# Optimization experiments

Measured on AMD Instinct MI355X. Metric: run time of the kernel, lower is better.

## Reference

```python
import jax, jax.numpy as jnp
import numpy as np

N_NODES = 50000
N_EDGES = 150000
F_IN = 128
D = 512
N_GRAPHS = 256
BN_EPS = 1e-5


def setup_inputs() -> dict:
    key = jax.random.key(0)
    ks = jax.random.split(key, 16)
    x = jax.random.normal(ks[0], (N_NODES, F_IN), dtype=jnp.float32)
    edge_index = jax.random.randint(ks[1], (2, N_EDGES), 0, N_NODES, dtype=jnp.int64)
    batch = jnp.sort(jax.random.randint(ks[2], (N_NODES,), 0, N_GRAPHS, dtype=jnp.int64))
    # layer 1 MLP (F_IN -> D -> D)
    W1a = jax.random.normal(ks[3], (F_IN, D), dtype=jnp.float32) / np.sqrt(F_IN)
    b1a = jnp.zeros((D,), dtype=jnp.float32)
    W1b = jax.random.normal(ks[4], (D, D), dtype=jnp.float32) / np.sqrt(D)
    b1b = jnp.zeros((D,), dtype=jnp.float32)
    # layers 2-5 MLPs (D -> D -> D), stacked on leading axis
    Wa = jax.random.normal(ks[5], (4, D, D), dtype=jnp.float32) / np.sqrt(D)
    ba = jnp.zeros((4, D), dtype=jnp.float32)
    Wb = jax.random.normal(ks[6], (4, D, D), dtype=jnp.float32) / np.sqrt(D)
    bb = jnp.zeros((4, D), dtype=jnp.float32)
    # batchnorm affine params for the 5 BN layers
    gammas = jnp.ones((5, D), dtype=jnp.float32)
    betas = jnp.zeros((5, D), dtype=jnp.float32)
    # final fc
    fcW = jax.random.normal(ks[7], (D, D), dtype=jnp.float32) / np.sqrt(D)
    fcb = jnp.zeros((D,), dtype=jnp.float32)
    return {"x": x, "edge_index": edge_index, "batch": batch,
            "W1a": W1a, "b1a": b1a, "W1b": W1b, "b1b": b1b,
            "Wa": Wa, "ba": ba, "Wb": Wb, "bb": bb,
            "gammas": gammas, "betas": betas, "fcW": fcW, "fcb": fcb}


def _gin_block(x, src, dst, wa, ba_, wb, bb_, gamma, beta):
    # GINConv (eps=0): h_i = x_i + sum_{j->i} x_j, then 2-layer MLP
    agg = jnp.zeros_like(x).at[dst].add(x[src])
    h = x + agg
    h = jnp.maximum(h @ wa + ba_, 0.0) @ wb + bb_
    # outer ReLU then BatchNorm1d (training-mode batch stats, biased var)
    h = jnp.maximum(h, 0.0)
    mean = h.mean(axis=0)
    var = ((h - mean) ** 2).mean(axis=0)
    return gamma * (h - mean) * jax.lax.rsqrt(var + BN_EPS) + beta


def reference(x, edge_index, batch, W1a, b1a, W1b, b1b, Wa, ba, Wb, bb,
              gammas, betas, fcW, fcb):
    src, dst = edge_index[0], edge_index[1]
    h = _gin_block(x, src, dst, W1a, b1a, W1b, b1b, gammas[0], betas[0])
    for i in range(4):
        h = _gin_block(h, src, dst, Wa[i], ba[i], Wb[i], bb[i],
                       gammas[i + 1], betas[i + 1])
    # global mean pool over graphs
    sums = jax.ops.segment_sum(h, batch, num_segments=N_GRAPHS)
    counts = jax.ops.segment_sum(jnp.ones((h.shape[0],), dtype=h.dtype), batch,
                                 num_segments=N_GRAPHS)
    pooled = sums / jnp.maximum(counts, 1.0)[:, None]
    return jnp.tanh(pooled @ fcW + fcb)
```

## Files before the change

kernel.cpp:

```cpp
#include <hip/hip_runtime.h>
#include <math.h>

typedef unsigned short u16;
typedef unsigned int u32;
typedef __attribute__((ext_vector_type(8))) short bf16x8;
typedef __attribute__((ext_vector_type(4))) float f32x4;

__device__ __forceinline__ u16 f2bf(float x) {
    u32 u = __float_as_uint(x);
    return (u16)((u + 0x7FFFu + ((u >> 16) & 1u)) >> 16);
}
__device__ __forceinline__ float bf2f(u16 h) {
    return __uint_as_float(((u32)h) << 16);
}
__device__ __forceinline__ void async16(const void* g, void* l) {
    __builtin_amdgcn_global_load_lds((const __attribute__((address_space(1))) void*)g,
                                     (__attribute__((address_space(3))) void*)l,
                                     16, 0, 0);
}

__device__ __forceinline__ int idx_at(const void* p, long long i, int is64) {
    if (is64) return (int)((const long long*)p)[i];
    return ((const int*)p)[i];
}

__global__ void detect_kernel(const int* __restrict__ ei, int E, int* __restrict__ flag) {
    __shared__ int any;
    if (threadIdx.x == 0) any = 0;
    __syncthreads();
    int n = min(E, 1024);
    for (int i = threadIdx.x; i < n; i += blockDim.x)
        if (ei[2 * i + 1] != 0) any = 1;
    __syncthreads();
    if (threadIdx.x == 0) *flag = (any == 0) ? 1 : 0;
}

__global__ void hist_kernel(const void* __restrict__ idx, long long offs,
                            const int* __restrict__ flag,
                            int* __restrict__ cnt, int n) {
    int is64 = *flag;
    int i = blockIdx.x * blockDim.x + threadIdx.x;
    if (i < n) atomicAdd(&cnt[idx_at(idx, offs + i, is64)], 1);
}

__global__ void scan1_kernel(const int* __restrict__ cnt, int* __restrict__ ofs,
                             int* __restrict__ bsum, int n) {
    __shared__ int s[256];
    int b = blockIdx.x, t = threadIdx.x;
    int base = b * 1024 + t * 4;
    int v0 = (base + 0 < n) ? cnt[base + 0] : 0;
    int v1 = (base + 1 < n) ? cnt[base + 1] : 0;
    int v2 = (base + 2 < n) ? cnt[base + 2] : 0;
    int v3 = (base + 3 < n) ? cnt[base + 3] : 0;
    int tsum = v0 + v1 + v2 + v3;
    s[t] = tsum;
    __syncthreads();
    for (int off = 1; off < 256; off <<= 1) {
        int u = (t >= off) ? s[t - off] : 0;
        __syncthreads();
        s[t] += u;
        __syncthreads();
    }
    int pre = s[t] - tsum;
    int e0 = pre + v0, e1 = e0 + v1, e2 = e1 + v2, e3 = e2 + v3;
    if (base + 0 < n) ofs[base + 1] = e0;
    if (base + 1 < n) ofs[base + 2] = e1;
    if (base + 2 < n) ofs[base + 3] = e2;
    if (base + 3 < n) ofs[base + 4] = e3;
    if (t == 255) bsum[b] = s[255];
    if (b == 0 && t == 0) ofs[0] = 0;
}

__global__ void scan2_kernel(int* __restrict__ bsum, int nb) {
    int t = threadIdx.x;
    int orig = (t < nb) ? bsum[t] : 0;
    int v = orig;
    for (int d = 1; d < 64; d <<= 1) {
        int u = __shfl_up(v, d);
        if (t >= d) v += u;
    }
    if (t < nb) bsum[t] = v - orig;
}

__global__ void scan3_kernel(int* __restrict__ ofs, const int* __restrict__ bsum, int n) {
    int i = blockIdx.x * blockDim.x + threadIdx.x;
    if (i < n) ofs[i + 1] += bsum[i >> 10];
}

__global__ void fill_csr_kernel(const void* __restrict__ ei, long long E,
                                const int* __restrict__ flag,
                                int* __restrict__ cursor, int* __restrict__ esrc, int e) {
    int is64 = *flag;
    int i = blockIdx.x * blockDim.x + threadIdx.x;
    if (i < e) {
        int d = idx_at(ei, E + i, is64);
        int s = idx_at(ei, i, is64);
        int p = atomicAdd(&cursor[d], 1);
        esrc[p] = s;
    }
}

__global__ void copy_int_kernel(const int* __restrict__ a, int* __restrict__ b, int n) {
    int i = blockIdx.x * blockDim.x + threadIdx.x;
    if (i < n) b[i] = a[i];
}

__global__ void aggregate_split_kernel(const float* __restrict__ X,
                                       const int* __restrict__ row_ofs,
                                       const int* __restrict__ esrc,
                                       const float* __restrict__ scale,
                                       const float* __restrict__ shift,
                                       u16* __restrict__ Zhi, u16* __restrict__ Zlo,
                                       int n, int ncols) {
    int tpr = ncols >> 2;
    int nper = 256 / tpr;
    int node = blockIdx.x * nper + threadIdx.x / tpr;
    int c = (threadIdx.x % tpr) * 4;
    if (node >= n) return;
    int beg = row_ofs[node], end = row_ofs[node + 1];
    float4 acc = *reinterpret_cast<const float4*>(X + (size_t)node * ncols + c);
    int e = beg;
    for (; e + 1 < end; e += 2) {
        int s0 = esrc[e], s1 = esrc[e + 1];
        float4 a = *reinterpret_cast<const float4*>(X + (size_t)s0 * ncols + c);
        float4 b = *reinterpret_cast<const float4*>(X + (size_t)s1 * ncols + c);
        acc.x += a.x + b.x; acc.y += a.y + b.y;
        acc.z += a.z + b.z; acc.w += a.w + b.w;
    }
    if (e < end) {
        int s0 = esrc[e];
        float4 a = *reinterpret_cast<const float4*>(X + (size_t)s0 * ncols + c);
        acc.x += a.x; acc.y += a.y; acc.z += a.z; acc.w += a.w;
    }
    if (scale) {
        float d1 = (float)(end - beg + 1);
        float4 sc = *reinterpret_cast<const float4*>(scale + c);
        float4 sh = *reinterpret_cast<const float4*>(shift + c);
        acc.x = sc.x * acc.x + d1 * sh.x;
        acc.y = sc.y * acc.y + d1 * sh.y;
        acc.z = sc.z * acc.z + d1 * sh.z;
        acc.w = sc.w * acc.w + d1 * sh.w;
    }
    ushort4 hv, lv;
    hv.x = f2bf(acc.x); lv.x = f2bf(acc.x - bf2f(hv.x));
    hv.y = f2bf(acc.y); lv.y = f2bf(acc.y - bf2f(hv.y));
    hv.z = f2bf(acc.z); lv.z = f2bf(acc.z - bf2f(hv.z));
    hv.w = f2bf(acc.w); lv.w = f2bf(acc.w - bf2f(hv.w));
    *reinterpret_cast<ushort4*>(Zhi + (size_t)node * ncols + c) = hv;
    *reinterpret_cast<ushort4*>(Zlo + (size_t)node * ncols + c) = lv;
}

__global__ void transpose_split_kernel(const float* __restrict__ W, int K, int N,
                                       u16* __restrict__ Thi, u16* __restrict__ Tlo) {
    __shared__ float t[32][33];
    int k0 = blockIdx.x * 32, n0 = blockIdx.y * 32;
    int tx = threadIdx.x & 31, ty = threadIdx.x >> 5;
#pragma unroll
    for (int i = 0; i < 32; i += 8)
        t[ty + i][tx] = W[(size_t)(k0 + ty + i) * N + n0 + tx];
    __syncthreads();
#pragma unroll
    for (int i = 0; i < 32; i += 8) {
        float v = t[tx][ty + i];
        size_t o = (size_t)(n0 + ty + i) * K + k0 + tx;
        u16 h = f2bf(v);
        Thi[o] = h;
        Tlo[o] = f2bf(v - bf2f(h));
    }
}

struct TBatch {
    const float* src[10];
    u16* dh[10];
    u16* dl[10];
};
__global__ void transpose_split_batch_kernel(TBatch tb) {
    __shared__ float t[32][33];
    int z = blockIdx.z;
    const float* W = tb.src[z];
    u16* Thi = tb.dh[z];
    u16* Tlo = tb.dl[z];
    int k0 = blockIdx.x * 32, n0 = blockIdx.y * 32;
    int tx = threadIdx.x & 31, ty = threadIdx.x >> 5;
#pragma unroll
    for (int i = 0; i < 32; i += 8)
        t[ty + i][tx] = W[(size_t)(k0 + ty + i) * 512 + n0 + tx];
    __syncthreads();
#pragma unroll
    for (int i = 0; i < 32; i += 8) {
        float v = t[tx][ty + i];
        size_t o = (size_t)(n0 + ty + i) * 512 + k0 + tx;
        u16 h = f2bf(v);
        Thi[o] = h;
        Tlo[o] = f2bf(v - bf2f(h));
    }
}

template <int MODE>
__global__ __launch_bounds__(512, 2)
void gemm_mfma(const u16* __restrict__ Ahi, const u16* __restrict__ Alo,
               const u16* __restrict__ Bhi, const u16* __restrict__ Blo,
               const float* __restrict__ bias, int M, int K, int mblk,
               u16* __restrict__ Ohi, u16* __restrict__ Olo,
               float* __restrict__ Of32, float* __restrict__ stats) {
    __shared__ __align__(16) char lds[131072];

    const int bid = blockIdx.x;
    const int mt = (bid >> 5) * 8 + (bid & 7);
    const int nbk = (bid & 31) >> 3;
    if (mt >= mblk) return;
    const int row0 = mt * 128;
    const int col0 = nbk * 128;

    const int tid = threadIdx.x;
    const int lane = tid & 63;
    const int wave = tid >> 6;
    const int wr = wave >> 2, wc = wave & 3;

    f32x4 acc[4][2];
#pragma unroll
    for (int mi = 0; mi < 4; ++mi)
#pragma unroll
        for (int ni = 0; ni < 2; ++ni)
            acc[mi][ni] = (f32x4){0.f, 0.f, 0.f, 0.f};

    auto stage = [&](int buf, int kt) {
        char* ldsA = lds + buf * 65536;
        char* ldsB = ldsA + 32768;
        const int k0 = kt << 6;
#pragma unroll
        for (int i = 0; i < 4; ++i) {
            int lin = tid + i * 512;
            int row = lin >> 4, p = lin & 15;
            int c = p ^ (row & 15);
            int eo = (c & 7) * 8;
            int ar = row0 + row; if (ar > M - 1) ar = M - 1;
            const u16* asrc = (c < 8 ? Ahi : Alo) + (size_t)ar * K + k0 + eo;
            async16(asrc, ldsA + lin * 16);
            const u16* bsrc = (c < 8 ? Bhi : Blo) + (size_t)(col0 + row) * K + k0 + eo;
            async16(bsrc, ldsB + lin * 16);
        }
    };

    const int nkt = K >> 6;
    stage(0, 0);
    __syncthreads();

    int cur = 0;
    for (int kt = 0; kt < nkt; ++kt) {
        if (kt + 1 < nkt) stage(cur ^ 1, kt + 1);
        char* ldsA = lds + cur * 65536;
        char* ldsB = ldsA + 32768;
#pragma unroll
        for (int kk = 0; kk < 2; ++kk) {
            bf16x8 ah[4], al[4], bh[2], bl[2];
            const int kc = lane >> 4;
            const int chi = kk * 4 + kc;
#pragma unroll
            for (int mi = 0; mi < 4; ++mi) {
                int ml = wr * 64 + mi * 16 + (lane & 15);
                const char* base = ldsA + ml * 256;
                ah[mi] = *(const bf16x8*)(base + ((chi ^ (ml & 15)) << 4));
                al[mi] = *(const bf16x8*)(base + (((chi + 8) ^ (ml & 15)) << 4));
            }
#pragma unroll
            for (int ni = 0; ni < 2; ++ni) {
                int nl = wc * 32 + ni * 16 + (lane & 15);
                const char* base = ldsB + nl * 256;
                bh[ni] = *(const bf16x8*)(base + ((chi ^ (nl & 15)) << 4));
                bl[ni] = *(const bf16x8*)(base + (((chi + 8) ^ (nl & 15)) << 4));
            }
            __builtin_amdgcn_s_setprio(1);
#pragma unroll
            for (int mi = 0; mi < 4; ++mi)
#pragma unroll
                for (int ni = 0; ni < 2; ++ni) {
                    acc[mi][ni] = __builtin_amdgcn_mfma_f32_16x16x32_bf16(
                        ah[mi], bh[ni], acc[mi][ni], 0, 0, 0);
                    acc[mi][ni] = __builtin_amdgcn_mfma_f32_16x16x32_bf16(
                        ah[mi], bl[ni], acc[mi][ni], 0, 0, 0);
                    acc[mi][ni] = __builtin_amdgcn_mfma_f32_16x16x32_bf16(
                        al[mi], bh[ni], acc[mi][ni], 0, 0, 0);
                }
            __builtin_amdgcn_s_setprio(0);
        }
        __syncthreads();
        cur ^= 1;
    }

    const int cl = lane & 15;
    const int rb = (lane >> 4) * 4;
    if (MODE == 0) {
#pragma unroll
        for (int ni = 0; ni < 2; ++ni) {
            int gc = col0 + wc * 32 + ni * 16 + cl;
            float bv = bias[gc];
#pragma unroll
            for (int mi = 0; mi < 4; ++mi) {
                int gr0 = row0 + wr * 64 + mi * 16 + rb;
#pragma unroll
                for (int r = 0; r < 4; ++r) {
                    int gr = gr0 + r;
                    if (gr < M) {
                        float v = fmaxf(acc[mi][ni][r] + bv, 0.f);
                        u16 h = f2bf(v);
                        Ohi[(size_t)gr * 512 + gc] = h;
                        Olo[(size_t)gr * 512 + gc] = f2bf(v - bf2f(h));
                    }
                }
            }
        }
    } else {
#pragma unroll
        for (int ni = 0; ni < 2; ++ni) {
            int gc = col0 + wc * 32 + ni * 16 + cl;
            float bv = bias[gc];
            float s = 0.f, q = 0.f;
#pragma unroll
            for (int mi = 0; mi < 4; ++mi) {
                int gr0 = row0 + wr * 64 + mi * 16 + rb;
#pragma unroll
                for (int r = 0; r < 4; ++r) {
                    int gr = gr0 + r;
                    if (gr < M) {
                        float v = fmaxf(acc[mi][ni][r] + bv, 0.f);
                        Of32[(size_t)gr * 512 + gc] = v;
                        s += v; q += v * v;
                    }
                }
            }
            s += __shfl_xor(s, 16); s += __shfl_xor(s, 32);
            q += __shfl_xor(q, 16); q += __shfl_xor(q, 32);
            if (lane < 16) {
                atomicAdd(&stats[gc], s);
                atomicAdd(&stats[512 + gc], q);
            }
        }
    }
}

__global__ void bn_params_kernel(const float* __restrict__ stats,
                                 const float* __restrict__ gamma,
                                 const float* __restrict__ beta,
                                 float* __restrict__ scale, float* __restrict__ shift,
                                 float invN) {
    int c = blockIdx.x * blockDim.x + threadIdx.x;
    if (c >= 512) return;
    float mean = stats[c] * invN;
    float var = fmaxf(stats[512 + c] * invN - mean * mean, 0.f);
    float a = gamma[c] * rsqrtf(var + 1e-5f);
    scale[c] = a;
    shift[c] = beta[c] - mean * a;
}

#define POOL_ROWS 64
__global__ void pool_kernel(const float* __restrict__ H, const void* __restrict__ batch,
                            const int* __restrict__ flag,
                            float* __restrict__ pooled, int n) {
    int is64 = *flag;
    int c = threadIdx.x * 4;
    int r0 = blockIdx.x * POOL_ROWS;
    if (r0 >= n) return;
    int r1 = min(r0 + POOL_ROWS, n);
    int g = idx_at(batch, r0, is64);
    float4 acc = make_float4(0.f, 0.f, 0.f, 0.f);
    for (int r = r0; r < r1; ++r) {
        int gr = idx_at(batch, r, is64);
        if (gr != g) {
            atomicAdd(&pooled[(size_t)g * 512 + c + 0], acc.x);
            atomicAdd(&pooled[(size_t)g * 512 + c + 1], acc.y);
            atomicAdd(&pooled[(size_t)g * 512 + c + 2], acc.z);
            atomicAdd(&pooled[(size_t)g * 512 + c + 3], acc.w);
            acc = make_float4(0.f, 0.f, 0.f, 0.f);
            g = gr;
        }
        float4 v = *reinterpret_cast<const float4*>(H + (size_t)r * 512 + c);
        acc.x += v.x; acc.y += v.y; acc.z += v.z; acc.w += v.w;
    }
    atomicAdd(&pooled[(size_t)g * 512 + c + 0], acc.x);
    atomicAdd(&pooled[(size_t)g * 512 + c + 1], acc.y);
    atomicAdd(&pooled[(size_t)g * 512 + c + 2], acc.z);
    atomicAdd(&pooled[(size_t)g * 512 + c + 3], acc.w);
}

__global__ void finalize_pool_kernel(const float* __restrict__ pooled,
                                     const int* __restrict__ cg,
                                     const float* __restrict__ scale,
                                     const float* __restrict__ shift,
                                     float* __restrict__ Apool, int total) {
    int idx = blockIdx.x * blockDim.x + threadIdx.x;
    if (idx >= total) return;
    int g = idx >> 9;
    int c = idx & 511;
    float cnt = fmaxf((float)cg[g], 1.f);
    Apool[idx] = scale[c] * (pooled[idx] / cnt) + shift[c];
}

__global__ void fc_tanh_kernel(const float* __restrict__ A,
                               const u16* __restrict__ WThi, const u16* __restrict__ WTlo,
                               const float* __restrict__ bias,
                               float* __restrict__ out, int G) {
    int tm = threadIdx.x >> 6;
    int tn = threadIdx.x & 63;
    int m = blockIdx.x * 4 + tm;
    int n = blockIdx.y * 64 + tn;
    if (m >= G) return;
    const float* a = A + (size_t)m * 512;
    const u16* wh = WThi + (size_t)n * 512;
    const u16* wl = WTlo + (size_t)n * 512;
    float acc = 0.f;
    for (int k = 0; k < 512; k += 4) {
        float4 av = *reinterpret_cast<const float4*>(a + k);
        ushort4 h4 = *reinterpret_cast<const ushort4*>(wh + k);
        ushort4 l4 = *reinterpret_cast<const ushort4*>(wl + k);
        acc += av.x * (bf2f(h4.x) + bf2f(l4.x));
        acc += av.y * (bf2f(h4.y) + bf2f(l4.y));
        acc += av.z * (bf2f(h4.z) + bf2f(l4.z));
        acc += av.w * (bf2f(h4.w) + bf2f(l4.w));
    }
    out[(size_t)m * 512 + n] = tanhf(acc + bias[n]);
}

extern "C" void kernel_launch(void* const* d_in, const int* in_sizes, int n_in,
                              void* d_out, int out_size, void* d_ws, size_t ws_size,
                              hipStream_t stream) {
    const float* x      = (const float*)d_in[0];
    const void*  ei     = d_in[1];
    const void*  batch  = d_in[2];
    const float* W1a    = (const float*)d_in[3];
    const float* b1a    = (const float*)d_in[4];
    const float* W1b    = (const float*)d_in[5];
    const float* b1b    = (const float*)d_in[6];
    const float* Wa     = (const float*)d_in[7];
    const float* ba     = (const float*)d_in[8];
    const float* Wb     = (const float*)d_in[9];
    const float* bb     = (const float*)d_in[10];
    const float* gammas = (const float*)d_in[11];
    const float* betas  = (const float*)d_in[12];
    const float* fcW    = (const float*)d_in[13];
    const float* fcb    = (const float*)d_in[14];

    const int N = in_sizes[2];
    const int E = in_sizes[1] / 2;
    const int F = in_sizes[0] / N;
    const int G = out_size / 512;

    char* w = (char*)d_ws;
    size_t off = 0;
    auto alloc = [&](size_t bytes) -> void* {
        void* p = w + off;
        off = (off + bytes + 255) & ~(size_t)255;
        return p;
    };
    float* slotA  = (float*)alloc((size_t)N * 512 * 4);
    float* slotB  = (float*)alloc((size_t)N * 512 * 4);
    int*   row_ofs= (int*)alloc((size_t)(N + 1) * 4);
    int*   cnt    = (int*)alloc((size_t)N * 4);
    int*   esrc   = (int*)alloc((size_t)E * 4);
    int*   cg     = (int*)alloc((size_t)G * 4);
    int*   bsum   = (int*)alloc(256 * 4);
    float* stats  = (float*)alloc(1024 * 4);
    float* scale  = (float*)alloc(512 * 4);
    float* shift  = (float*)alloc(512 * 4);
    float* pooled = (float*)alloc((size_t)G * 512 * 4);
    float* Apool  = (float*)alloc((size_t)G * 512 * 4);
    int*   flag   = (int*)alloc(256);
    const size_t WSZ = (size_t)512 * 512;
    u16* g1h[5]; u16* g1l[5]; u16* g2h[5]; u16* g2l[5];
    for (int i = 0; i < 5; ++i) {
        g1h[i] = (u16*)alloc(WSZ * 2); g1l[i] = (u16*)alloc(WSZ * 2);
        g2h[i] = (u16*)alloc(WSZ * 2); g2l[i] = (u16*)alloc(WSZ * 2);
    }
    u16* fch = (u16*)alloc(WSZ * 2); u16* fcl = (u16*)alloc(WSZ * 2);
    (void)ws_size; (void)n_in;

    {
        dim3 gK128(128 / 32, 512 / 32);
        transpose_split_kernel<<<gK128, 256, 0, stream>>>(W1a, 128, 512, g1h[0], g1l[0]);
        TBatch tb;
        tb.src[0] = W1b; tb.dh[0] = g2h[0]; tb.dl[0] = g2l[0];
        for (int i = 0; i < 4; ++i) {
            tb.src[1 + i] = Wa + (size_t)i * WSZ; tb.dh[1 + i] = g1h[i + 1]; tb.dl[1 + i] = g1l[i + 1];
            tb.src[5 + i] = Wb + (size_t)i * WSZ; tb.dh[5 + i] = g2h[i + 1]; tb.dl[5 + i] = g2l[i + 1];
        }
        tb.src[9] = fcW; tb.dh[9] = fch; tb.dl[9] = fcl;
        dim3 gB(16, 16, 10);
        transpose_split_batch_kernel<<<gB, 256, 0, stream>>>(tb);
    }

    detect_kernel<<<1, 256, 0, stream>>>((const int*)ei, E, flag);
    hipMemsetAsync(cnt, 0, (size_t)N * 4, stream);
    hist_kernel<<<(E + 255) / 256, 256, 0, stream>>>(ei, (long long)E, flag, cnt, E);
    int nb = (N + 1023) / 1024;
    scan1_kernel<<<nb, 256, 0, stream>>>(cnt, row_ofs, bsum, N);
    scan2_kernel<<<1, 64, 0, stream>>>(bsum, nb);
    scan3_kernel<<<(N + 255) / 256, 256, 0, stream>>>(row_ofs, bsum, N);
    copy_int_kernel<<<(N + 255) / 256, 256, 0, stream>>>(row_ofs, cnt, N);
    fill_csr_kernel<<<(E + 255) / 256, 256, 0, stream>>>(ei, (long long)E, flag, cnt, esrc, E);
    hipMemsetAsync(cg, 0, (size_t)G * 4, stream);
    hist_kernel<<<(N + 255) / 256, 256, 0, stream>>>(batch, 0, flag, cg, N);

    const float* curH = x;
    float* zslot = slotA;
    float* tslot = slotB;
    int ncols = F;
    const float* scaleP = nullptr;
    const float* shiftP = nullptr;
    const int mblk = (N + 127) / 128;
    const int ngrp = (mblk + 7) / 8;
    dim3 ggrid(ngrp * 32);

    for (int L = 0; L < 5; ++L) {
        u16* Zhi = (u16*)zslot; u16* Zlo = Zhi + (size_t)N * 512;
        u16* Thi = (u16*)tslot; u16* Tlo = Thi + (size_t)N * 512;
        float* H = zslot;

        int tpr = ncols / 4;
        int nper = 256 / tpr;
        aggregate_split_kernel<<<(N + nper - 1) / nper, 256, 0, stream>>>(
            curH, row_ofs, esrc, scaleP, shiftP, Zhi, Zlo, N, ncols);

        const float* ba_ = (L == 0) ? b1a : ba + (size_t)(L - 1) * 512;
        const float* bb_ = (L == 0) ? b1b : bb + (size_t)(L - 1) * 512;

        gemm_mfma<0><<<ggrid, 512, 0, stream>>>(Zhi, Zlo, g1h[L], g1l[L], ba_,
                                                N, ncols, mblk, Thi, Tlo, nullptr, nullptr);
        hipMemsetAsync(stats, 0, 1024 * 4, stream);
        gemm_mfma<1><<<ggrid, 512, 0, stream>>>(Thi, Tlo, g2h[L], g2l[L], bb_,
                                                N, 512, mblk, nullptr, nullptr, H, stats);
        bn_params_kernel<<<2, 256, 0, stream>>>(stats, gammas + (size_t)L * 512,
                                                betas + (size_t)L * 512,
                                                scale, shift, 1.f / (float)N);
        curH = H;
        ncols = 512;
        scaleP = scale;
        shiftP = shift;
        float* tmp = zslot; zslot = tslot; tslot = tmp;
    }
    const float* Hfin = curH;

    hipMemsetAsync(pooled, 0, (size_t)G * 512 * 4, stream);
    pool_kernel<<<(N + POOL_ROWS - 1) / POOL_ROWS, 128, 0, stream>>>(Hfin, batch, flag, pooled, N);
    int total = G * 512;
    finalize_pool_kernel<<<(total + 255) / 256, 256, 0, stream>>>(pooled, cg, scale, shift,
                                                                  Apool, total);

    dim3 fgrid((G + 3) / 4, 512 / 64);
    fc_tanh_kernel<<<fgrid, 256, 0, stream>>>(Apool, fch, fcl, fcb, (float*)d_out, G);
}
```

Before: 1.703 ms.

## Switch GEMM to 32x32x16 MFMA with 4 waves and single-buffered LDS

Rewrites the split-bf16 GEMM to use 32x32x16 MFMA instructions, 256-thread blocks where each of 4 waves computes a 64x64 sub-tile, and a single 64KB LDS buffer instead of double buffering. Larger MFMA tiles reduce the LDS reads per flop and the instruction count. Dropping the double buffer halves LDS use, which may let more blocks share a CU, but the global loads for each k-step no longer overlap with compute.

New measurement: 1.737 ms. About the same (+2.0%).

```diff
diff --git a/kernel.cpp b/kernel.cpp
--- a/kernel.cpp
+++ b/kernel.cpp
@@ -4,7 +4,7 @@
 typedef unsigned short u16;
 typedef unsigned int u32;
 typedef __attribute__((ext_vector_type(8))) short bf16x8;
-typedef __attribute__((ext_vector_type(4))) float f32x4;
+typedef __attribute__((ext_vector_type(16))) float f32x16;
 
 __device__ __forceinline__ u16 f2bf(float x) {
     u32 u = __float_as_uint(x);
@@ -197,13 +197,15 @@
 }
 
 template <int MODE>
-__global__ __launch_bounds__(512, 2)
+__global__ __launch_bounds__(256, 2)
 void gemm_mfma(const u16* __restrict__ Ahi, const u16* __restrict__ Alo,
                const u16* __restrict__ Bhi, const u16* __restrict__ Blo,
                const float* __restrict__ bias, int M, int K, int mblk,
                u16* __restrict__ Ohi, u16* __restrict__ Olo,
                float* __restrict__ Of32, float* __restrict__ stats) {
-    __shared__ __align__(16) char lds[131072];
+    __shared__ __align__(16) char lds[65536];
+    char* ldsA = lds;
+    char* ldsB = lds + 32768;
 
     const int bid = blockIdx.x;
     const int mt = (bid >> 5) * 8 + (bid & 7);
@@ -215,22 +217,22 @@
     const int tid = threadIdx.x;
     const int lane = tid & 63;
     const int wave = tid >> 6;
-    const int wr = wave >> 2, wc = wave & 3;
-
-    f32x4 acc[4][2];
-#pragma unroll
-    for (int mi = 0; mi < 4; ++mi)
+    const int wr = wave >> 1, wc = wave & 1;
+
+    f32x16 acc[2][2];
+#pragma unroll
+    for (int mi = 0; mi < 2; ++mi)
 #pragma unroll
         for (int ni = 0; ni < 2; ++ni)
-            acc[mi][ni] = (f32x4){0.f, 0.f, 0.f, 0.f};
-
-    auto stage = [&](int buf, int kt) {
-        char* ldsA = lds + buf * 65536;
-        char* ldsB = ldsA + 32768;
+#pragma unroll
+            for (int r = 0; r < 16; ++r) acc[mi][ni][r] = 0.f;
+
+    const int nkt = K >> 6;
+    for (int kt = 0; kt < nkt; ++kt) {
         const int k0 = kt << 6;
 #pragma unroll
-        for (int i = 0; i < 4; ++i) {
-            int lin = tid + i * 512;
+        for (int i = 0; i < 8; ++i) {
+            int lin = tid + i * 256;
             int row = lin >> 4, p = lin & 15;
             int c = p ^ (row & 15);
             int eo = (c & 7) * 8;
@@ -240,67 +242,55 @@
             const u16* bsrc = (c < 8 ? Bhi : Blo) + (size_t)(col0 + row) * K + k0 + eo;
             async16(bsrc, ldsB + lin * 16);
         }
-    };
-
-    const int nkt = K >> 6;
-    stage(0, 0);
-    __syncthreads();
-
-    int cur = 0;
-    for (int kt = 0; kt < nkt; ++kt) {
-        if (kt + 1 < nkt) stage(cur ^ 1, kt + 1);
-        char* ldsA = lds + cur * 65536;
-        char* ldsB = ldsA + 32768;
-#pragma unroll
-        for (int kk = 0; kk < 2; ++kk) {
-            bf16x8 ah[4], al[4], bh[2], bl[2];
-            const int kc = lane >> 4;
-            const int chi = kk * 4 + kc;
-#pragma unroll
-            for (int mi = 0; mi < 4; ++mi) {
-                int ml = wr * 64 + mi * 16 + (lane & 15);
+        __syncthreads();
+#pragma unroll
+        for (int ks = 0; ks < 4; ++ks) {
+            bf16x8 ah[2], al[2], bh[2], bl[2];
+            const int ch = ks * 2 + (lane >> 5);
+#pragma unroll
+            for (int mi = 0; mi < 2; ++mi) {
+                int ml = wr * 64 + mi * 32 + (lane & 31);
                 const char* base = ldsA + ml * 256;
-                ah[mi] = *(const bf16x8*)(base + ((chi ^ (ml & 15)) << 4));
-                al[mi] = *(const bf16x8*)(base + (((chi + 8) ^ (ml & 15)) << 4));
+                ah[mi] = *(const bf16x8*)(base + ((ch ^ (ml & 15)) << 4));
+                al[mi] = *(const bf16x8*)(base + (((ch + 8) ^ (ml & 15)) << 4));
             }
 #pragma unroll
             for (int ni = 0; ni < 2; ++ni) {
-                int nl = wc * 32 + ni * 16 + (lane & 15);
+                int nl = wc * 64 + ni * 32 + (lane & 31);
                 const char* base = ldsB + nl * 256;
-                bh[ni] = *(const bf16x8*)(base + ((chi ^ (nl & 15)) << 4));
-                bl[ni] = *(const bf16x8*)(base + (((chi + 8) ^ (nl & 15)) << 4));
+                bh[ni] = *(const bf16x8*)(base + ((ch ^ (nl & 15)) << 4));
+                bl[ni] = *(const bf16x8*)(base + (((ch + 8) ^ (nl & 15)) << 4));
             }
             __builtin_amdgcn_s_setprio(1);
 #pragma unroll
-            for (int mi = 0; mi < 4; ++mi)
+            for (int mi = 0; mi < 2; ++mi)
 #pragma unroll
                 for (int ni = 0; ni < 2; ++ni) {
-                    acc[mi][ni] = __builtin_amdgcn_mfma_f32_16x16x32_bf16(
+                    acc[mi][ni] = __builtin_amdgcn_mfma_f32_32x32x16_bf16(
                         ah[mi], bh[ni], acc[mi][ni], 0, 0, 0);
-                    acc[mi][ni] = __builtin_amdgcn_mfma_f32_16x16x32_bf16(
+                    acc[mi][ni] = __builtin_amdgcn_mfma_f32_32x32x16_bf16(
                         ah[mi], bl[ni], acc[mi][ni], 0, 0, 0);
-                    acc[mi][ni] = __builtin_amdgcn_mfma_f32_16x16x32_bf16(
+                    acc[mi][ni] = __builtin_amdgcn_mfma_f32_32x32x16_bf16(
                         al[mi], bh[ni], acc[mi][ni], 0, 0, 0);
                 }
             __builtin_amdgcn_s_setprio(0);
         }
         __syncthreads();
-        cur ^= 1;
-    }
-
-    const int cl = lane & 15;
-    const int rb = (lane >> 4) * 4;
+    }
+
+    const int cl = lane & 31;
+    const int r4 = (lane >> 5) * 4;
     if (MODE == 0) {
 #pragma unroll
         for (int ni = 0; ni < 2; ++ni) {
-            int gc = col0 + wc * 32 + ni * 16 + cl;
+            int gc = col0 + wc * 64 + ni * 32 + cl;
             float bv = bias[gc];
 #pragma unroll
-            for (int mi = 0; mi < 4; ++mi) {
-                int gr0 = row0 + wr * 64 + mi * 16 + rb;
-#pragma unroll
-                for (int r = 0; r < 4; ++r) {
-                    int gr = gr0 + r;
+            for (int mi = 0; mi < 2; ++mi) {
+                int gr0 = row0 + wr * 64 + mi * 32 + r4;
+#pragma unroll
+                for (int r = 0; r < 16; ++r) {
+                    int gr = gr0 + (r & 3) + 8 * (r >> 2);
                     if (gr < M) {
                         float v = fmaxf(acc[mi][ni][r] + bv, 0.f);
                         u16 h = f2bf(v);
@@ -313,15 +303,15 @@
     } else {
 #pragma unroll
         for (int ni = 0; ni < 2; ++ni) {
-            int gc = col0 + wc * 32 + ni * 16 + cl;
+            int gc = col0 + wc * 64 + ni * 32 + cl;
             float bv = bias[gc];
             float s = 0.f, q = 0.f;
 #pragma unroll
-            for (int mi = 0; mi < 4; ++mi) {
-                int gr0 = row0 + wr * 64 + mi * 16 + rb;
-#pragma unroll
-                for (int r = 0; r < 4; ++r) {
-                    int gr = gr0 + r;
+            for (int mi = 0; mi < 2; ++mi) {
+                int gr0 = row0 + wr * 64 + mi * 32 + r4;
+#pragma unroll
+                for (int r = 0; r < 16; ++r) {
+                    int gr = gr0 + (r & 3) + 8 * (r >> 2);
                     if (gr < M) {
                         float v = fmaxf(acc[mi][ni][r] + bv, 0.f);
                         Of32[(size_t)gr * 512 + gc] = v;
@@ -329,9 +319,9 @@
                     }
                 }
             }
-            s += __shfl_xor(s, 16); s += __shfl_xor(s, 32);
-            q += __shfl_xor(q, 16); q += __shfl_xor(q, 32);
-            if (lane < 16) {
+            s += __shfl_xor(s, 32);
+            q += __shfl_xor(q, 32);
+            if (lane < 32) {
                 atomicAdd(&stats[gc], s);
                 atomicAdd(&stats[512 + gc], q);
             }
@@ -523,10 +513,10 @@
         const float* ba_ = (L == 0) ? b1a : ba + (size_t)(L - 1) * 512;
         const float* bb_ = (L == 0) ? b1b : bb + (size_t)(L - 1) * 512;
 
-        gemm_mfma<0><<<ggrid, 512, 0, stream>>>(Zhi, Zlo, g1h[L], g1l[L], ba_,
+        gemm_mfma<0><<<ggrid, 256, 0, stream>>>(Zhi, Zlo, g1h[L], g1l[L], ba_,
                                                 N, ncols, mblk, Thi, Tlo, nullptr, nullptr);
         hipMemsetAsync(stats, 0, 1024 * 4, stream);
-        gemm_mfma<1><<<ggrid, 512, 0, stream>>>(Thi, Tlo, g2h[L], g2l[L], bb_,
+        gemm_mfma<1><<<ggrid, 256, 0, stream>>>(Thi, Tlo, g2h[L], g2l[L], bb_,
                                                 N, 512, mblk, nullptr, nullptr, H, stats);
         bn_params_kernel<<<2, 256, 0, stream>>>(stats, gammas + (size_t)L * 512,
                                                 betas + (size_t)L * 512,
```
